# Kernel optimization log

Hardware: AMD Instinct MI355X
Metric: run time of the kernel (lower is better)

Reference implementation:

```python
import jax, jax.numpy as jnp
import numpy as np

B, T, NC, WD, UNITS = 128, 256, 128, 512, 512
IN_DIM = NC + WD + NC  # x_char + x_word + one-hot prev word


def setup_inputs() -> dict:
    key = jax.random.key(0)
    ks = jax.random.split(key, 7)
    scale = 0.05  # keep gates out of saturation
    return {
        "x_char": jax.random.normal(ks[0], (B, T, NC), jnp.float32),
        "x_word": jax.random.normal(ks[1], (B, T, WD), jnp.float32),
        "W": jax.random.normal(ks[2], (IN_DIM, 4 * UNITS), jnp.float32) * scale,
        "U": jax.random.normal(ks[3], (UNITS, 4 * UNITS), jnp.float32) * scale,
        "b": jnp.zeros((4 * UNITS,), jnp.float32),
        "Ws": jax.random.normal(ks[4], (UNITS, NC), jnp.float32) * scale,
        "bs": jnp.zeros((NC,), jnp.float32),
    }


def reference(x_char, x_word, W, U, b, Ws, bs):
    Bsz, Tlen, nclasses = x_char.shape
    units = U.shape[0]
    # time-major, concat char+word features (matches x_shuffled in original)
    x_t = jnp.concatenate(
        [jnp.swapaxes(x_char, 0, 1), jnp.swapaxes(x_word, 0, 1)], axis=-1
    )  # [T, B, NC+WD]
    word0 = jnp.full((Bsz, nclasses), 1e-5, x_char.dtype)  # start_char
    h0 = jnp.zeros((Bsz, units), x_char.dtype)
    c0 = jnp.zeros((Bsz, units), x_char.dtype)

    def step(carry, x_i):
        word_vec, h, c = carry
        ins = jnp.concatenate([x_i, word_vec], axis=1)  # [B, IN_DIM]
        z = ins @ W + h @ U + b  # [B, 4*units]; Keras gate order i,f,c,o
        zi, zf, zg, zo = jnp.split(z, 4, axis=1)
        i = jax.nn.sigmoid(zi)
        f = jax.nn.sigmoid(zf)
        g = jnp.tanh(zg)
        o = jax.nn.sigmoid(zo)
        c_new = f * c + i * g
        h_new = o * jnp.tanh(c_new)
        probs = jax.nn.softmax(h_new @ Ws + bs, axis=-1)
        idx = jnp.argmax(probs, axis=1)  # [B]
        word_vec_new = jax.nn.one_hot(idx, nclasses, dtype=x_char.dtype)
        return (word_vec_new, h_new, c_new), idx

    _, idxs = jax.lax.scan(step, (word0, h0, c0), x_t)  # idxs: [T, B]
    return jnp.swapaxes(idxs, 0, 1)  # [B, T] int word indices
```

## Files before the change

kernel.cpp:

```cpp
#include <hip/hip_runtime.h>
#include <math.h>

#define BSZ   128
#define TLEN  256
#define NCLS  128
#define WDIM  512
#define XDIM  640
#define G4    2048

#define BT    16
#define JTS   16
#define NBLK  256
#define NTHR  512
#define KCH   8

#define H_OFF    0
#define LOG_OFF  131072
#define W0_OFF   180224
#define FLAG_OFF 182272

typedef unsigned long long ull;

__device__ __forceinline__ float sigmoidf_(float x) {
  return 1.0f / (1.0f + expf(-x));
}

__device__ __forceinline__ float4 ld_dev16(const float* p) {
  const ull* q = (const ull*)p;
  ull a = __hip_atomic_load(q,     __ATOMIC_RELAXED, __HIP_MEMORY_SCOPE_AGENT);
  ull b = __hip_atomic_load(q + 1, __ATOMIC_RELAXED, __HIP_MEMORY_SCOPE_AGENT);
  float4 r;
  ((ull*)&r)[0] = a;
  ((ull*)&r)[1] = b;
  return r;
}

__global__ void setup_kernel(const float* __restrict__ W,
                             const float* __restrict__ bias,
                             float* __restrict__ ws) {
  int tid = blockIdx.x * blockDim.x + threadIdx.x;
  for (int i = tid; i < 3 * BSZ * NCLS; i += 64 * 256)
    ws[LOG_OFF + i] = 0.0f;
  if (tid < 4096)
    ((unsigned int*)(ws + FLAG_OFF))[tid] = 0u;
  if (tid < G4) {
    float s = 0.0f;
    #pragma unroll 4
    for (int r = 0; r < NCLS; ++r)
      s += W[(size_t)(XDIM + r) * G4 + tid];
    ws[W0_OFF + tid] = bias[tid] + 1e-5f * s;
  }
}

__global__ void __launch_bounds__(NTHR, 1)
lstm_main(const float* __restrict__ xc, const float* __restrict__ xw,
          const float* __restrict__ W,  const float* __restrict__ U,
          const float* __restrict__ bias, const float* __restrict__ Wsm,
          const float* __restrict__ bsv, int* __restrict__ out,
          float* __restrict__ ws)
{
  __shared__ float U_lds[512 * 64];
  __shared__ float ins_lds[2][2176];
  __shared__ float wsm_lds[16 * 128];
  __shared__ float hl_lds[16 * 17];
  __shared__ int   idx_lds[BT];

  float* zred  = &ins_lds[0][0];
  float* Wt    = &ins_lds[0][0];
  float* red_v = zred;
  int*   red_i = (int*)(zred + 528);

  const int tid = threadIdx.x;
  const int blk = blockIdx.x;
  const int grp = blk & 7;
  const int jt  = blk >> 3;
  const int b0  = grp * BT;
  const int j0  = jt * JTS;

  const int gb  = tid & 15;
  const int gg  = (tid >> 4) & 3;
  const int j4  = (tid >> 6) & 3;
  const int kh  = tid >> 8;
  const int c0  = gg * 512 + j0 + j4 * 4;
  const int cc0 = gg * 16 + j4 * 4;

  const int srow = tid >> 5;
  const int sseg = tid & 31;

  const int ub = tid >> 5;
  const int um = tid & 31;

  const int vb = (tid >> 4) & 15;
  const int vj = tid & 15;

  float* hbuf   = ws + H_OFF;
  float* logits = ws + LOG_OFF;
  unsigned int* flags = (unsigned int*)(ws + FLAG_OFF);
  unsigned int* myflag   = flags + (grp * 32 + jt) * 16;
  unsigned int* pollflag = flags + (grp * 32 + (tid & 31)) * 16;

  {
    int cc  = tid & 63;
    int col = (cc >> 4) * 512 + j0 + (cc & 15);
    int k0  = tid >> 6;
    for (int kk = 0; kk < 64; ++kk) {
      int k = kk * 8 + k0;
      U_lds[k * 64 + cc] = U[(size_t)k * G4 + col];
    }
  }
  {
    int row = tid >> 5, col4 = tid & 31;
    *(float4*)(&wsm_lds[row * 128 + col4 * 4]) =
        *(const float4*)(Wsm + (size_t)(j0 + row) * NCLS + col4 * 4);
  }

  float4 xq[KCH];
  auto chunk_gemm = [&](int tt0) {
    #pragma unroll
    for (int s = 0; s < KCH; ++s) xq[s] = make_float4(0.f, 0.f, 0.f, 0.f);
    #pragma unroll 1
    for (int kt = 0; kt < 10; ++kt) {
      int id0 = tid,       k0t = id0 >> 4, cg0 = id0 & 15;
      int id1 = tid + 512, k1t = id1 >> 4, cg1 = id1 & 15;
      int col0 = (cg0 >> 2) * 512 + j0 + (cg0 & 3) * 4;
      int col1 = (cg1 >> 2) * 512 + j0 + (cg1 & 3) * 4;
      float4 wv0 = *(const float4*)(W + (size_t)(kt * 64 + k0t) * G4 + col0);
      float4 wv1 = *(const float4*)(W + (size_t)(kt * 64 + k1t) * G4 + col1);
      __syncthreads();
      *(float4*)(Wt + k0t * 64 + cg0 * 4) = wv0;
      *(float4*)(Wt + k1t * 64 + cg1 * 4) = wv1;
      __syncthreads();
      const float* wp = Wt + (kh * 32) * 64 + cc0;
      const float* xb0 = (kt < 2)
        ? xc + ((size_t)(b0 + gb) * TLEN + tt0) * NCLS + kt * 64 + kh * 32
        : xw + ((size_t)(b0 + gb) * TLEN + tt0) * WDIM + (kt * 64 - 128) + kh * 32;
      const size_t xstr = (kt < 2) ? (size_t)NCLS : (size_t)WDIM;
      #pragma unroll
      for (int sb = 0; sb < 2; ++sb) {
        #pragma unroll 1
        for (int q = 0; q < 8; ++q) {
          const float* wq = wp + q * 4 * 64;
          float4 w0 = *(const float4*)(wq);
          float4 w1 = *(const float4*)(wq + 64);
          float4 w2 = *(const float4*)(wq + 128);
          float4 w3 = *(const float4*)(wq + 192);
          const float* xquad = xb0 + (size_t)(sb * 4) * xstr + q * 4;
          #pragma unroll
          for (int u = 0; u < 4; ++u) {
            const int s = sb * 4 + u;
            float4 xa = *(const float4*)(xquad + (size_t)u * xstr);
            xq[s].x = fmaf(xa.x, w0.x, xq[s].x);
            xq[s].y = fmaf(xa.x, w0.y, xq[s].y);
            xq[s].z = fmaf(xa.x, w0.z, xq[s].z);
            xq[s].w = fmaf(xa.x, w0.w, xq[s].w);
            xq[s].x = fmaf(xa.y, w1.x, xq[s].x);
            xq[s].y = fmaf(xa.y, w1.y, xq[s].y);
            xq[s].z = fmaf(xa.y, w1.z, xq[s].z);
            xq[s].w = fmaf(xa.y, w1.w, xq[s].w);
            xq[s].x = fmaf(xa.z, w2.x, xq[s].x);
            xq[s].y = fmaf(xa.z, w2.y, xq[s].y);
            xq[s].z = fmaf(xa.z, w2.z, xq[s].z);
            xq[s].w = fmaf(xa.z, w2.w, xq[s].w);
            xq[s].x = fmaf(xa.w, w3.x, xq[s].x);
            xq[s].y = fmaf(xa.w, w3.y, xq[s].y);
            xq[s].z = fmaf(xa.w, w3.z, xq[s].z);
            xq[s].w = fmaf(xa.w, w3.w, xq[s].w);
          }
          __builtin_amdgcn_sched_barrier(0);
        }
      }
    }
  };

  float creg = 0.0f;

  __syncthreads();
  chunk_gemm(0);
  __syncthreads();

  for (int t = 0; t < TLEN; ++t) {
    float4 acc = xq[0];
    #pragma unroll
    for (int s = 0; s < KCH - 1; ++s) xq[s] = xq[s + 1];

    if (t == 0) {
      if (kh == 0) {
        const float4 w0 = *(const float4*)(ws + W0_OFF + c0);
        acc.x += w0.x; acc.y += w0.y; acc.z += w0.z; acc.w += w0.w;
      }
    } else {
      {
        const float* lsrc = logits + ((t + 2) % 3) * (BSZ * NCLS)
                          + (b0 + ub) * NCLS + um * 4;
        const float4 bb = *(const float4*)(bsv + um * 4);
        float4 lv = ld_dev16(lsrc);
        float bv = lv.x + bb.x; int bi = um * 4;
        if (lv.y + bb.y > bv) { bv = lv.y + bb.y; bi = um * 4 + 1; }
        if (lv.z + bb.z > bv) { bv = lv.z + bb.z; bi = um * 4 + 2; }
        if (lv.w + bb.w > bv) { bv = lv.w + bb.w; bi = um * 4 + 3; }
        red_v[ub * 33 + um] = bv; red_i[ub * 33 + um] = bi;
        float* lz = logits + ((t + 1) % 3) * (BSZ * NCLS) + b0 * NCLS;
        if (tid < 64)
          __hip_atomic_store(&lz[jt * 64 + tid], 0.0f,
                             __ATOMIC_RELAXED, __HIP_MEMORY_SCOPE_AGENT);
        __syncthreads();
        if (um == 0) {
          float v = red_v[ub * 33]; int vi = red_i[ub * 33];
          #pragma unroll
          for (int s = 1; s < 32; ++s) {
            float v2 = red_v[ub * 33 + s];
            int   i2 = red_i[ub * 33 + s];
            if (v2 > v || (v2 == v && i2 < vi)) { v = v2; vi = i2; }
          }
          idx_lds[ub] = vi;
          if (jt == 0) out[(b0 + ub) * TLEN + (t - 1)] = vi;
        }
        __syncthreads();
      }
      if (kh == 0) {
        int wr = XDIM + idx_lds[gb];
        const float4 b4 = *(const float4*)(bias + c0);
        const float4 w4 = *(const float4*)(W + (size_t)wr * G4 + c0);
        acc.x += b4.x + w4.x;  acc.y += b4.y + w4.y;
        acc.z += b4.z + w4.z;  acc.w += b4.w + w4.w;
      }
      {
        const float* hprev = hbuf + ((t + 1) & 1) * (BSZ * 512);
        {
          float4 r = ld_dev16(hprev + (size_t)(b0 + srow) * 512 + sseg * 4);
          *(float4*)(&ins_lds[0][srow * 132 + sseg * 4]) = r;
          __syncthreads();
        }
        #pragma unroll 1
        for (int ch = 0; ch < 4; ++ch) {
          float4 nxt;
          if (ch + 1 < 4) {
            nxt = ld_dev16(hprev + (size_t)(b0 + srow) * 512
                           + (ch + 1) * 128 + sseg * 4);
          }
          const float* up = U_lds + (ch * 128 + kh * 64) * 64 + cc0;
          const float* ip = &ins_lds[ch & 1][gb * 132 + kh * 64];
          #pragma unroll 8
          for (int kk = 0; kk < 64; ++kk) {
            float a = ip[kk];
            float4 u4 = *(const float4*)(up + kk * 64);
            acc.x = fmaf(a, u4.x, acc.x);
            acc.y = fmaf(a, u4.y, acc.y);
            acc.z = fmaf(a, u4.z, acc.z);
            acc.w = fmaf(a, u4.w, acc.w);
          }
          if (ch + 1 < 4) {
            *(float4*)(&ins_lds[(ch + 1) & 1][srow * 132 + sseg * 4]) = nxt;
            __syncthreads();
          }
        }
      }
    }

    *(float4*)(zred + (gb * 2 + kh) * 68 + cc0) = acc;
    __syncthreads();

    if (tid < 256) {
      float zi = zred[(vb * 2) * 68 +  0 + vj] + zred[(vb * 2 + 1) * 68 +  0 + vj];
      float zf = zred[(vb * 2) * 68 + 16 + vj] + zred[(vb * 2 + 1) * 68 + 16 + vj];
      float zg = zred[(vb * 2) * 68 + 32 + vj] + zred[(vb * 2 + 1) * 68 + 32 + vj];
      float zo = zred[(vb * 2) * 68 + 48 + vj] + zred[(vb * 2 + 1) * 68 + 48 + vj];
      float iv = sigmoidf_(zi);
      float fv = sigmoidf_(zf);
      float gv = tanhf(zg);
      float ov = sigmoidf_(zo);
      creg = fv * creg + iv * gv;
      float hn = ov * tanhf(creg);
      __hip_atomic_store(hbuf + (t & 1) * (BSZ * 512)
                         + (size_t)(b0 + vb) * 512 + j0 + vj, hn,
                         __ATOMIC_RELAXED, __HIP_MEMORY_SCOPE_AGENT);
      hl_lds[vb * 17 + vj] = hn;
    }
    __syncthreads();

    {
      float p0 = 0.f, p1 = 0.f, p2 = 0.f, p3 = 0.f;
      #pragma unroll
      for (int j = 0; j < 16; ++j) {
        float hv = hl_lds[ub * 17 + j];
        const float4 wv = *(const float4*)(&wsm_lds[j * 128 + um * 4]);
        p0 = fmaf(hv, wv.x, p0); p1 = fmaf(hv, wv.y, p1);
        p2 = fmaf(hv, wv.z, p2); p3 = fmaf(hv, wv.w, p3);
      }
      float* ld = logits + (t % 3) * (BSZ * NCLS)
                + (size_t)(b0 + ub) * NCLS + um * 4;
      atomicAdd(ld + 0, p0); atomicAdd(ld + 1, p1);
      atomicAdd(ld + 2, p2); atomicAdd(ld + 3, p3);
    }

    __syncthreads();
    if (tid == 0)
      __hip_atomic_store(myflag, (unsigned)(t + 1),
                         __ATOMIC_RELAXED, __HIP_MEMORY_SCOPE_AGENT);
    if (((t + 1) & (KCH - 1)) == 0 && t + 1 < TLEN)
      chunk_gemm(t + 1);
    if (tid < 64) {
      const unsigned tgt = (unsigned)(t + 1);
      for (;;) {
        unsigned v = __hip_atomic_load(pollflag, __ATOMIC_RELAXED,
                                       __HIP_MEMORY_SCOPE_AGENT);
        if (__all(v >= tgt)) break;
        __builtin_amdgcn_s_sleep(1);
      }
    }
    __syncthreads();
  }

  if (jt == 0) {
    const float* lsrc = logits + ((TLEN - 1) % 3) * (BSZ * NCLS)
                      + (b0 + ub) * NCLS + um * 4;
    const float4 bb = *(const float4*)(bsv + um * 4);
    float4 lv = ld_dev16(lsrc);
    float bv = lv.x + bb.x; int bi = um * 4;
    if (lv.y + bb.y > bv) { bv = lv.y + bb.y; bi = um * 4 + 1; }
    if (lv.z + bb.z > bv) { bv = lv.z + bb.z; bi = um * 4 + 2; }
    if (lv.w + bb.w > bv) { bv = lv.w + bb.w; bi = um * 4 + 3; }
    __syncthreads();
    red_v[ub * 33 + um] = bv; red_i[ub * 33 + um] = bi;
    __syncthreads();
    if (um == 0) {
      float v = red_v[ub * 33]; int vi = red_i[ub * 33];
      #pragma unroll
      for (int s = 1; s < 32; ++s) {
        float v2 = red_v[ub * 33 + s];
        int   i2 = red_i[ub * 33 + s];
        if (v2 > v || (v2 == v && i2 < vi)) { v = v2; vi = i2; }
      }
      out[(b0 + ub) * TLEN + (TLEN - 1)] = vi;
    }
  }
}

extern "C" void kernel_launch(void* const* d_in, const int* in_sizes, int n_in,
                              void* d_out, int out_size, void* d_ws, size_t ws_size,
                              hipStream_t stream) {
  (void)in_sizes; (void)n_in; (void)out_size; (void)ws_size;
  const float* xc  = (const float*)d_in[0];
  const float* xw  = (const float*)d_in[1];
  const float* W   = (const float*)d_in[2];
  const float* U   = (const float*)d_in[3];
  const float* b   = (const float*)d_in[4];
  const float* Wsm = (const float*)d_in[5];
  const float* bs  = (const float*)d_in[6];
  int*   out = (int*)d_out;
  float* ws  = (float*)d_ws;

  hipLaunchKernelGGL(setup_kernel, dim3(64), dim3(256), 0, stream, W, b, ws);

  void* args[] = { (void*)&xc, (void*)&xw, (void*)&W, (void*)&U, (void*)&b,
                   (void*)&Wsm, (void*)&bs, (void*)&out, (void*)&ws };
  hipLaunchCooperativeKernel((const void*)lstm_main, dim3(NBLK), dim3(NTHR),
                             args, 0, stream);
}
```

Measured before the change: 8.829 ms.

## Replace atomicAdd logit accumulation with per-block partials reduced by readers

Each of the 32 column-tile blocks in a batch group now stores its partial logits to its own double-buffered slot with plain device-scope stores, instead of doing float atomicAdds into a shared triple-buffered logits array. At the next step every block sums the 32 partials itself before taking the argmax. This removes contended global atomics and the per-step zeroing of the next buffer. In exchange each block reads 32 partials per step (more global read traffic, done redundantly by all blocks), and the partials use a much larger workspace.

Result: slower. 9.126 ms (+3.4%).

```diff
diff --git a/kernel.cpp b/kernel.cpp
--- a/kernel.cpp
+++ b/kernel.cpp
@@ -14,10 +14,10 @@
 #define NTHR  512
 #define KCH   8
 
-#define H_OFF    0
-#define LOG_OFF  131072
-#define W0_OFF   180224
-#define FLAG_OFF 182272
+#define H_OFF     0
+#define LPART_OFF 131072
+#define W0_OFF    1179648
+#define FLAG_OFF  1181696
 
 typedef unsigned long long ull;
 
@@ -35,12 +35,16 @@
   return r;
 }
 
+__device__ __forceinline__ void st_dev16(float* p, float4 v) {
+  ull* q = (ull*)p;
+  __hip_atomic_store(q,     ((ull*)&v)[0], __ATOMIC_RELAXED, __HIP_MEMORY_SCOPE_AGENT);
+  __hip_atomic_store(q + 1, ((ull*)&v)[1], __ATOMIC_RELAXED, __HIP_MEMORY_SCOPE_AGENT);
+}
+
 __global__ void setup_kernel(const float* __restrict__ W,
                              const float* __restrict__ bias,
                              float* __restrict__ ws) {
   int tid = blockIdx.x * blockDim.x + threadIdx.x;
-  for (int i = tid; i < 3 * BSZ * NCLS; i += 64 * 256)
-    ws[LOG_OFF + i] = 0.0f;
   if (tid < 4096)
     ((unsigned int*)(ws + FLAG_OFF))[tid] = 0u;
   if (tid < G4) {
@@ -94,7 +98,7 @@
   const int vj = tid & 15;
 
   float* hbuf   = ws + H_OFF;
-  float* logits = ws + LOG_OFF;
+  float* lpart  = ws + LPART_OFF;
   unsigned int* flags = (unsigned int*)(ws + FLAG_OFF);
   unsigned int* myflag   = flags + (grp * 32 + jt) * 16;
   unsigned int* pollflag = flags + (grp * 32 + (tid & 31)) * 16;
@@ -190,19 +194,33 @@
       }
     } else {
       {
-        const float* lsrc = logits + ((t + 2) % 3) * (BSZ * NCLS)
-                          + (b0 + ub) * NCLS + um * 4;
+        const float* pb = lpart
+            + (((size_t)((t - 1) & 1) * NBLK) + grp * 32) * (BT * NCLS)
+            + (size_t)ub * NCLS + um * 4;
+        float4 s0 = make_float4(0.f, 0.f, 0.f, 0.f);
+        float4 s1 = s0, s2 = s0, s3 = s0;
+        #pragma unroll 1
+        for (int j2 = 0; j2 < 32; j2 += 4) {
+          float4 a = ld_dev16(pb + (size_t)(j2 + 0) * (BT * NCLS));
+          float4 b = ld_dev16(pb + (size_t)(j2 + 1) * (BT * NCLS));
+          float4 c = ld_dev16(pb + (size_t)(j2 + 2) * (BT * NCLS));
+          float4 d = ld_dev16(pb + (size_t)(j2 + 3) * (BT * NCLS));
+          s0.x += a.x; s0.y += a.y; s0.z += a.z; s0.w += a.w;
+          s1.x += b.x; s1.y += b.y; s1.z += b.z; s1.w += b.w;
+          s2.x += c.x; s2.y += c.y; s2.z += c.z; s2.w += c.w;
+          s3.x += d.x; s3.y += d.y; s3.z += d.z; s3.w += d.w;
+        }
+        float4 lv;
+        lv.x = (s0.x + s1.x) + (s2.x + s3.x);
+        lv.y = (s0.y + s1.y) + (s2.y + s3.y);
+        lv.z = (s0.z + s1.z) + (s2.z + s3.z);
+        lv.w = (s0.w + s1.w) + (s2.w + s3.w);
         const float4 bb = *(const float4*)(bsv + um * 4);
-        float4 lv = ld_dev16(lsrc);
         float bv = lv.x + bb.x; int bi = um * 4;
         if (lv.y + bb.y > bv) { bv = lv.y + bb.y; bi = um * 4 + 1; }
         if (lv.z + bb.z > bv) { bv = lv.z + bb.z; bi = um * 4 + 2; }
         if (lv.w + bb.w > bv) { bv = lv.w + bb.w; bi = um * 4 + 3; }
         red_v[ub * 33 + um] = bv; red_i[ub * 33 + um] = bi;
-        float* lz = logits + ((t + 1) % 3) * (BSZ * NCLS) + b0 * NCLS;
-        if (tid < 64)
-          __hip_atomic_store(&lz[jt * 64 + tid], 0.0f,
-                             __ATOMIC_RELAXED, __HIP_MEMORY_SCOPE_AGENT);
         __syncthreads();
         if (um == 0) {
           float v = red_v[ub * 33]; int vi = red_i[ub * 33];
@@ -287,10 +305,10 @@
         p0 = fmaf(hv, wv.x, p0); p1 = fmaf(hv, wv.y, p1);
         p2 = fmaf(hv, wv.z, p2); p3 = fmaf(hv, wv.w, p3);
       }
-      float* ld = logits + (t % 3) * (BSZ * NCLS)
-                + (size_t)(b0 + ub) * NCLS + um * 4;
-      atomicAdd(ld + 0, p0); atomicAdd(ld + 1, p1);
-      atomicAdd(ld + 2, p2); atomicAdd(ld + 3, p3);
+      float* dst = lpart
+          + (((size_t)(t & 1) * NBLK) + (grp * 32 + jt)) * (BT * NCLS)
+          + (size_t)ub * NCLS + um * 4;
+      st_dev16(dst, make_float4(p0, p1, p2, p3));
     }
 
     __syncthreads();
@@ -312,10 +330,28 @@
   }
 
   if (jt == 0) {
-    const float* lsrc = logits + ((TLEN - 1) % 3) * (BSZ * NCLS)
-                      + (b0 + ub) * NCLS + um * 4;
+    const float* pb = lpart
+        + (((size_t)((TLEN - 1) & 1) * NBLK) + grp * 32) * (BT * NCLS)
+        + (size_t)ub * NCLS + um * 4;
+    float4 s0 = make_float4(0.f, 0.f, 0.f, 0.f);
+    float4 s1 = s0, s2 = s0, s3 = s0;
+    #pragma unroll 1
+    for (int j2 = 0; j2 < 32; j2 += 4) {
+      float4 a = ld_dev16(pb + (size_t)(j2 + 0) * (BT * NCLS));
+      float4 b = ld_dev16(pb + (size_t)(j2 + 1) * (BT * NCLS));
+      float4 c = ld_dev16(pb + (size_t)(j2 + 2) * (BT * NCLS));
+      float4 d = ld_dev16(pb + (size_t)(j2 + 3) * (BT * NCLS));
+      s0.x += a.x; s0.y += a.y; s0.z += a.z; s0.w += a.w;
+      s1.x += b.x; s1.y += b.y; s1.z += b.z; s1.w += b.w;
+      s2.x += c.x; s2.y += c.y; s2.z += c.z; s2.w += c.w;
+      s3.x += d.x; s3.y += d.y; s3.z += d.z; s3.w += d.w;
+    }
+    float4 lv;
+    lv.x = (s0.x + s1.x) + (s2.x + s3.x);
+    lv.y = (s0.y + s1.y) + (s2.y + s3.y);
+    lv.z = (s0.z + s1.z) + (s2.z + s3.z);
+    lv.w = (s0.w + s1.w) + (s2.w + s3.w);
     const float4 bb = *(const float4*)(bsv + um * 4);
-    float4 lv = ld_dev16(lsrc);
     float bv = lv.x + bb.x; int bi = um * 4;
     if (lv.y + bb.y > bv) { bv = lv.y + bb.y; bi = um * 4 + 1; }
     if (lv.z + bb.z > bv) { bv = lv.z + bb.z; bi = um * 4 + 2; }
```
